# Optimization experiments

Measured on AMD Instinct MI355X. Metric: run time of the kernel, lower is better.

Reference implementation:

```python
import jax, jax.numpy as jnp
import numpy as np
from jax import lax

SR = 16000
N_FFT = 400
HOP = 200
N_MELS = 128
HID = 128


def _mel_fb():
    # torchaudio melscale_fbanks defaults: htk scale, norm=None, f_min=0, f_max=sr/2
    all_freqs = np.linspace(0.0, SR / 2, N_FFT // 2 + 1)  # (201,)
    hz2mel = lambda f: 2595.0 * np.log10(1.0 + f / 700.0)
    mel2hz = lambda m: 700.0 * (10.0 ** (m / 2595.0) - 1.0)
    m_pts = np.linspace(hz2mel(0.0), hz2mel(SR / 2), N_MELS + 2)
    f_pts = mel2hz(m_pts)  # (130,)
    f_diff = np.diff(f_pts)  # (129,)
    slopes = f_pts[None, :] - all_freqs[:, None]  # (201,130)
    down = -slopes[:, :-2] / f_diff[:-1]
    up = slopes[:, 2:] / f_diff[1:]
    fb = np.maximum(0.0, np.minimum(down, up))  # (201,128)
    return jnp.asarray(fb, dtype=jnp.float32)

MEL_FB = _mel_fb()
HANN = jnp.asarray(np.hanning(N_FFT + 1)[:-1], dtype=jnp.float32)  # periodic hann(400)


def mel_spectrogram(x):
    # x: (B, T) waveform -> (B, n_mels, frames), power=2 mel spectrogram
    pad = N_FFT // 2
    xp = jnp.pad(x, ((0, 0), (pad, pad)), mode='reflect')
    n_frames = 1 + (xp.shape[1] - N_FFT) // HOP  # 81 for T=16000
    idx = jnp.arange(n_frames)[:, None] * HOP + jnp.arange(N_FFT)[None, :]
    frames = xp[:, idx] * HANN  # (B, frames, 400)
    spec = jnp.fft.rfft(frames, axis=-1)  # (B, frames, 201)
    power = jnp.abs(spec) ** 2
    mel = power @ MEL_FB  # (B, frames, 128)
    return jnp.transpose(mel, (0, 2, 1))  # (B, 128, frames)


def lstm_layer(x, W, U, b):
    # x: (B, T, F); gate order i, f, g, o (matches torch slicing)
    B = x.shape[0]
    h0 = jnp.zeros((B, HID), x.dtype)
    c0 = jnp.zeros((B, HID), x.dtype)

    def step(carry, x_t):
        h, c = carry
        gates = x_t @ W + h @ U + b  # (B, 4H)
        i = jax.nn.sigmoid(gates[:, :HID])
        f = jax.nn.sigmoid(gates[:, HID:2 * HID])
        g = jnp.tanh(gates[:, 2 * HID:3 * HID])
        o = jax.nn.sigmoid(gates[:, 3 * HID:])
        c = f * c + i * g
        h = o * jnp.tanh(c)
        return (h, c), h

    _, hs = lax.scan(step, (h0, c0), jnp.transpose(x, (1, 0, 2)))  # (T, B, H)
    return jnp.transpose(hs, (1, 0, 2))  # (B, T, H)


def setup_inputs() -> dict:
    key = jax.random.key(0)
    ks = jax.random.split(key, 16)
    s = 0.05
    return {
        'x': jax.random.normal(ks[0], (1024, 16000), dtype=jnp.float32),
        'conv_w': jax.random.normal(ks[1], (128, 128, 3), dtype=jnp.float32) * s,  # (out,in,k)
        'conv_b': jax.random.normal(ks[2], (128,), dtype=jnp.float32) * s,
        'W1': jax.random.normal(ks[3], (128, 4 * HID), dtype=jnp.float32) * s,
        'U1': jax.random.normal(ks[4], (HID, 4 * HID), dtype=jnp.float32) * s,
        'b1': jax.random.normal(ks[5], (4 * HID,), dtype=jnp.float32) * s,
        'W2': jax.random.normal(ks[6], (HID, 4 * HID), dtype=jnp.float32) * s,
        'U2': jax.random.normal(ks[7], (HID, 4 * HID), dtype=jnp.float32) * s,
        'b2': jax.random.normal(ks[8], (4 * HID,), dtype=jnp.float32) * s,
        'fc1_w': jax.random.normal(ks[9], (128, 128), dtype=jnp.float32) * s,  # (in,out)
        'fc1_b': jax.random.normal(ks[10], (128,), dtype=jnp.float32) * s,
        'proj_w': jax.random.normal(ks[11], (128, 35), dtype=jnp.float32) * s,  # (in,out)
        'proj_b': jax.random.normal(ks[12], (35,), dtype=jnp.float32) * s,
    }


def reference(x, conv_w, conv_b, W1, U1, b1, W2, U2, b2, fc1_w, fc1_b, proj_w, proj_b):
    # MelSpectrogram -> Conv1d(128,128,3) -> permute -> LSTM x2 -> fc1 -> mean(time) -> proj
    spec = mel_spectrogram(x)  # (B, 128, 81)
    conv = lax.conv_general_dilated(
        spec, conv_w, window_strides=(1,), padding='VALID',
        dimension_numbers=('NCH', 'OIH', 'NCH')) + conv_b[None, :, None]  # (B,128,79)
    h = jnp.transpose(conv, (0, 2, 1))  # (B, 79, 128)
    h = lstm_layer(h, W1, U1, b1)
    h = lstm_layer(h, W2, U2, b2)
    h = h @ fc1_w + fc1_b  # (B, 79, 128)
    h = jnp.mean(h, axis=1)  # (B, 128)
    return h @ proj_w + proj_b  # (B, 35)
```

## Files before the change

### kernel.cpp

```cpp
#include <hip/hip_runtime.h>
#include <math.h>

#define PI_D 3.14159265358979323846

#define BATCH   1024
#define TLEN    16000
#define NFFT    400
#define HOP     200
#define NFRAME  81
#define NBIN    201
#define NMEL    128
#define HID     128
#define TSTEPS  79
#define GATES   512

#define KDFT    416
#define NDFT    512
#define SINOFF  256
#define KPOW    224
#define KCONV   384
#define NCHUNK  2
#define CHROWS  (BATCH*NFRAME/NCHUNK)

static inline size_t al512(size_t v){ return (v + 511) & ~((size_t)511); }

__device__ __forceinline__ unsigned short bf_rne(float f){
    unsigned u = __float_as_uint(f);
    u += 0x7FFF + ((u >> 16) & 1);
    return (unsigned short)(u >> 16);
}
__device__ __forceinline__ void bf_split(float f, unsigned short& h, unsigned short& l){
    h = bf_rne(f);
    float hf = __uint_as_float(((unsigned)h) << 16);
    l = bf_rne(f - hf);
}
__device__ __forceinline__ void bf_split_fast(float f, unsigned short& h, unsigned short& l){
    unsigned u = __float_as_uint(f);
    h = (unsigned short)(u >> 16);
    float hf = __uint_as_float(u & 0xFFFF0000u);
    l = (unsigned short)(__float_as_uint(f - hf) >> 16);
}

__device__ __forceinline__ int kswz(int n, int k){
    return (k & ~31) | (((((k >> 3) & 3) ^ ((n >> 1) & 3))) << 3) | (k & 7);
}

typedef short bf16x8 __attribute__((ext_vector_type(8)));
typedef float f32x4  __attribute__((ext_vector_type(4)));
typedef unsigned short us8 __attribute__((ext_vector_type(8)));
typedef unsigned short us4 __attribute__((ext_vector_type(4)));
typedef _Float16 f16x8 __attribute__((ext_vector_type(8)));

__device__ __forceinline__ void gld16(const unsigned short* g, unsigned short* l){
    __builtin_amdgcn_global_load_lds(
        (const __attribute__((address_space(1))) unsigned int*)g,
        (__attribute__((address_space(3))) unsigned int*)l, 16, 0, 0);
}

__global__ void setup_dft_t(unsigned short* __restrict__ th, unsigned short* __restrict__ tl){
    int idx = blockIdx.x*256 + threadIdx.x;
    if (idx >= NDFT*KDFT) return;
    int n = idx / KDFT, k = idx % KDFT;
    double v = 0.0;
    if (k < 400) {
        double w = 0.5 - 0.5*cos(2.0*PI_D*(double)k/400.0);
        if (n < NBIN)                              v = w * cos(2.0*PI_D*(double)((k*n)%400)/400.0);
        else if (n >= SINOFF && n < SINOFF + NBIN) v = w * sin(2.0*PI_D*(double)((k*(n-SINOFF))%400)/400.0);
    }
    unsigned short h, l; bf_split((float)v, h, l);
    int o = n*KDFT + kswz(n, k);
    th[o] = h; tl[o] = l;
}

__global__ void setup_fb_t(unsigned short* __restrict__ fh, unsigned short* __restrict__ fl){
    int idx = blockIdx.x*256 + threadIdx.x;
    if (idx >= NMEL*KPOW) return;
    int m = idx / KPOW, f = idx % KPOW;
    float v = 0.f;
    if (f < NBIN) {
        double melmax = 2595.0 * log10(1.0 + 8000.0/700.0);
        double p0 = 700.0*(pow(10.0, melmax*(double)(m  )/129.0/2595.0) - 1.0);
        double p1 = 700.0*(pow(10.0, melmax*(double)(m+1)/129.0/2595.0) - 1.0);
        double p2 = 700.0*(pow(10.0, melmax*(double)(m+2)/129.0/2595.0) - 1.0);
        double freq = 40.0 * (double)f;
        double dn = (freq - p0)/(p1 - p0);
        double up = (p2 - freq)/(p2 - p1);
        double t  = dn < up ? dn : up;
        if (t < 0.0) t = 0.0;
        v = (float)t;
    }
    unsigned short h, l; bf_split(v, h, l);
    int o = m*KPOW + kswz(m, f);
    fh[o] = h; fl[o] = l;
}

__global__ void setup_wc_t(unsigned short* __restrict__ wh, unsigned short* __restrict__ wl,
                           const float* __restrict__ cw){
    int idx = blockIdx.x*256 + threadIdx.x;
    if (idx >= NMEL*KCONV) return;
    int o = idx / KCONV, kk = idx % KCONV;
    int ksh = kk >> 7, i = kk & 127;
    unsigned short h, l; bf_split(cw[o*384 + i*3 + ksh], h, l);
    int p = o*KCONV + kswz(o, kk);
    wh[p] = h; wl[p] = l;
}

__global__ void setup_w_t(unsigned short* __restrict__ wh, unsigned short* __restrict__ wl,
                          const float* __restrict__ w){
    int idx = blockIdx.x*256 + threadIdx.x;
    if (idx >= GATES*HID) return;
    int c = idx / HID, i = idx % HID;
    unsigned short h, l; bf_split(w[(size_t)i*GATES + c], h, l);
    int p = c*HID + kswz(c, i);
    wh[p] = h; wl[p] = l;
}

__global__ void setup_comb(float* __restrict__ cwm, float* __restrict__ cb,
                           const float* __restrict__ fc1w, const float* __restrict__ fc1b,
                           const float* __restrict__ projw, const float* __restrict__ projb){
    int idx = blockIdx.x*256 + threadIdx.x;
    if (idx < 128*64) {
        int i = idx / 64, o = idx % 64;
        float v = 0.f;
        if (o < 35) {
            double s = 0.0;
            for (int m = 0; m < 128; m++) s += (double)fc1w[i*128+m] * (double)projw[m*35+o];
            v = (float)s;
        }
        cwm[idx] = v;
    } else if (idx < 128*64 + 64) {
        int o = idx - 128*64;
        float v = 0.f;
        if (o < 35) {
            double s = (double)projb[o];
            for (int m = 0; m < 128; m++) s += (double)fc1b[m] * (double)projw[m*35+o];
            v = (float)s;
        }
        cb[o] = v;
    }
}

__global__ void setup_uf(_Float16* __restrict__ uf, const float* __restrict__ u){
    int idx = blockIdx.x*256 + threadIdx.x;
    if (idx >= 65536) return;
    int j    = idx & 7;
    int lane = (idx >> 3) & 63;
    int nt   = (idx >> 9) & 3;
    int ks   = (idx >> 11) & 3;
    int w    = (idx >> 13) & 7;
    int k = ks*32 + (lane >> 4)*8 + j;
    int c = w*64 + nt*16 + (lane & 15);
    uf[idx] = (_Float16)u[(size_t)k*GATES + c];
}

enum AMode { A_NORMAL=0, A_FRAMES=1, A_POWER=2, A_CONV3=3 };

template<int AMODE, bool BIAS, int NT>
__global__ __launch_bounds__(256)
void mgemm_k(const float* __restrict__ A,
             const unsigned short* __restrict__ BTh, const unsigned short* __restrict__ BTl,
             const float* __restrict__ bias, float* __restrict__ C,
             int Ksteps, int lda, int kstride, int ldc,
             const float* __restrict__ aux, int rowbase)
{
    __shared__ unsigned short Ash[2][128][32], Asl[2][128][32];
    __shared__ unsigned short Bsh[2][128][32], Bsl[2][128][32];

    const int nwg = gridDim.x;
    const int qq = nwg >> 3, rmd = nwg & 7;
    const int xcd = blockIdx.x & 7, loc = blockIdx.x >> 3;
    const int swz = (xcd < rmd ? xcd*(qq+1) : rmd*(qq+1) + (xcd - rmd)*qq) + loc;
    constexpr int LGNT = (NT == 4) ? 2 : 0;
    const int m0 = (swz >> LGNT) * 128;
    const int n0 = (swz & (NT-1)) * 128;

    const int tid = threadIdx.x;
    const int lane = tid & 63, w = tid >> 6;
    const int wr = (w >> 1) * 64, wc = (w & 1) * 64;
    const int l15 = lane & 15;
    const int swf = ((lane & 15) >> 1) & 3;
    const int pos = (((lane >> 4) ^ swf) << 3);

    const int sr  = tid >> 3;
    const int wcol = (((((tid & 7) >> 1)) ^ ((tid >> 4) & 3)) << 3) + ((tid & 1) << 2);

    float va0[16], vb0[16], va1[16], vb1[16];

    auto issue_loads = [&](float (&va)[16], float (&vb)[16], int ksn){
        const int k0n = ksn * 32;
        #pragma unroll
        for (int p = 0; p < 4; p++) {
            const int row = p*32 + sr;
            const int kk = k0n + (tid & 7)*4;
            if constexpr (AMODE == A_NORMAL) {
                *(float4*)&va[p*4] = *(const float4*)(A + (size_t)(m0+row)*lda + kk);
            } else if constexpr (AMODE == A_POWER) {
                const float* src = A + (size_t)(m0+row)*lda + kk;
                *(float4*)&va[p*4] = *(const float4*)(src);
                *(float4*)&vb[p*4] = *(const float4*)(src + SINOFF);
            } else if constexpr (AMODE == A_FRAMES) {
                const int rr = rowbase + m0 + row;
                const int b = rr / NFRAME, f = rr - b*NFRAME;
                const float* xb = aux + (size_t)b * TLEN;
                const int q0 = f*HOP + kk - 200;
                if (q0 >= 0 && q0 + 3 < TLEN) {
                    *(float4*)&va[p*4] = *(const float4*)(xb + q0);
                } else {
                    #pragma unroll
                    for (int j = 0; j < 4; j++) {
                        int q = q0 + j;
                        if (q < 0) q = -q;
                        else if (q >= TLEN) q = 2*TLEN - 2 - q;
                        va[p*4+j] = xb[q];
                    }
                }
            } else {
                const int rr = m0 + row;
                const int b = rr / TSTEPS, t = rr - b*TSTEPS;
                const int ksh = kk >> 7, i = kk & 127;
                *(float4*)&va[p*4] = *(const float4*)(aux + ((size_t)(b*NFRAME + t + ksh)*NMEL + i));
            }
        }
        (void)vb;
    };
    auto write_stage = [&](float (&va)[16], float (&vb)[16], int wb){
        #pragma unroll
        for (int p = 0; p < 4; p++) {
            const int row = p*32 + sr;
            us4 hv, lv;
            #pragma unroll
            for (int j = 0; j < 4; j++) {
                float f = va[p*4+j];
                if constexpr (AMODE == A_POWER) f = f*f + vb[p*4+j]*vb[p*4+j];
                unsigned short h, l; bf_split_fast(f, h, l);
                hv[j] = h; lv[j] = l;
            }
            *(us4*)&Ash[wb][row][wcol] = hv;
            *(us4*)&Asl[wb][row][wcol] = lv;
        }
        (void)vb;
    };
    auto dma_b = [&](int wb, int ksn){
        const int k0n = ksn * 32;
        #pragma unroll
        for (int p = 0; p < 2; p++) {
            const size_t o = (size_t)(n0 + p*64 + w*16 + (lane >> 2))*kstride + k0n + (lane & 3)*8;
            gld16(BTh + o, &Bsh[wb][p*64 + w*16][0]);
            gld16(BTl + o, &Bsl[wb][p*64 + w*16][0]);
        }
    };

    f32x4 acc[4][4] = {};

    issue_loads(va1, vb1, 0);
    dma_b(0, 0);
    write_stage(va1, vb1, 0);
    issue_loads(va0, vb0, 1);
    __syncthreads();

    auto iter = [&](int ks, float (&vac)[16], float (&vbc)[16],
                    float (&vao)[16], float (&vbo)[16], int bufc){
        const bool pf1 = (ks + 1 < Ksteps);
        const bool pf2 = (ks + 2 < Ksteps);
        if (pf2) issue_loads(vao, vbo, ks + 2);
        if (pf1) dma_b(bufc ^ 1, ks + 1);

        bf16x8 ah[4], al[4];
        #pragma unroll
        for (int mt = 0; mt < 4; mt++) {
            ah[mt] = *(const bf16x8*)&Ash[bufc][wr + mt*16 + l15][pos];
            al[mt] = *(const bf16x8*)&Asl[bufc][wr + mt*16 + l15][pos];
        }
        #pragma unroll
        for (int nt = 0; nt < 4; nt++) {
            const int nr = wc + nt*16 + l15;
            bf16x8 bh = *(const bf16x8*)&Bsh[bufc][nr][pos];
            bf16x8 bl = *(const bf16x8*)&Bsl[bufc][nr][pos];
            #pragma unroll
            for (int mt = 0; mt < 4; mt++) {
                acc[mt][nt] = __builtin_amdgcn_mfma_f32_16x16x32_bf16(ah[mt], bh, acc[mt][nt], 0, 0, 0);
                acc[mt][nt] = __builtin_amdgcn_mfma_f32_16x16x32_bf16(ah[mt], bl, acc[mt][nt], 0, 0, 0);
                acc[mt][nt] = __builtin_amdgcn_mfma_f32_16x16x32_bf16(al[mt], bh, acc[mt][nt], 0, 0, 0);
            }
        }

        if (pf1) {
            write_stage(vac, vbc, bufc ^ 1);
            __syncthreads();
        }
    };

    for (int ks = 0; ks < Ksteps; ks += 2) {
        iter(ks, va0, vb0, va1, vb1, 0);
        if (ks + 1 < Ksteps) iter(ks + 1, va1, vb1, va0, vb0, 1);
    }

    const int quad = lane >> 4;
    #pragma unroll
    for (int nt = 0; nt < 4; nt++) {
        const int col = n0 + wc + (nt << 4) + l15;
        float b = 0.f;
        if constexpr (BIAS) b = bias[col];
        #pragma unroll
        for (int mt = 0; mt < 4; mt++) {
            #pragma unroll
            for (int r = 0; r < 4; r++) {
                const int row = m0 + wr + (mt << 4) + quad*4 + r;
                C[(size_t)row*ldc + col] = acc[mt][nt][r] + b;
            }
        }
    }
}

__global__ __launch_bounds__(256)
void gemm_small(const float* __restrict__ A, const float* __restrict__ Bm,
                const float* __restrict__ bias, float* __restrict__ C,
                int M, int N, int K, int lda, int ldb, int ldc)
{
    __shared__ float As[16][64+4];
    __shared__ float Bs[16][64];
    const int tid = threadIdx.x;
    const int tx = tid & 15, ty = tid >> 4;
    const int m0 = blockIdx.x * 64;
    float acc[4][4] = {{0,0,0,0},{0,0,0,0},{0,0,0,0},{0,0,0,0}};
    const int am = tid >> 2, ak = (tid & 3) * 4;
    const int bk = tid >> 4, bn = (tid & 15) * 4;
    for (int k0 = 0; k0 < K; k0 += 16) {
        float4 av = *(const float4*)(A + (size_t)(m0+am)*lda + k0 + ak);
        As[ak+0][am]=av.x; As[ak+1][am]=av.y; As[ak+2][am]=av.z; As[ak+3][am]=av.w;
        *(float4*)&Bs[bk][bn] = *(const float4*)(Bm + (size_t)(k0+bk)*ldb + bn);
        __syncthreads();
        #pragma unroll
        for (int k = 0; k < 16; k++) {
            float4 a = *(const float4*)&As[k][ty*4];
            float4 b = *(const float4*)&Bs[k][tx*4];
            #pragma unroll
            for (int i = 0; i < 4; i++) {
                float av_ = ((const float*)&a)[i];
                acc[i][0] = fmaf(av_, b.x, acc[i][0]);
                acc[i][1] = fmaf(av_, b.y, acc[i][1]);
                acc[i][2] = fmaf(av_, b.z, acc[i][2]);
                acc[i][3] = fmaf(av_, b.w, acc[i][3]);
            }
        }
        __syncthreads();
    }
    #pragma unroll
    for (int ir = 0; ir < 4; ir++) {
        const int row = m0 + ty*4 + ir;
        #pragma unroll
        for (int jc = 0; jc < 4; jc++) {
            const int col = tx*4 + jc;
            if (col < N) C[(size_t)row*ldc + col] = acc[ir][jc] + bias[col];
        }
    }
}

__device__ __forceinline__ float sigm_f(float x){ return 1.f/(1.f + __expf(-x)); }
__device__ __forceinline__ float tanh_f(float x){ float e = __expf(2.f*x); return 1.f - 2.f/(e + 1.f); }

#define LROWS 4
#define LTHREADS 512
#define HPAD 136

__global__ __launch_bounds__(LTHREADS, 2)
void lstm_k(const float* __restrict__ X, const _Float16* __restrict__ Uf, float* __restrict__ H)
{
    __shared__ _Float16 hsA[16*HPAD];
    __shared__ float gs[GATES*5];
    const int tid = threadIdx.x;
    const int b0 = blockIdx.x * LROWS;
    const int lane = tid & 63, w = tid >> 6;
    const int m16 = lane & 15, quad = lane >> 4;
    const int r = tid >> 7;
    const int j = tid & 127;

    f32x4 bfr[4][4];
    #pragma unroll
    for (int ks = 0; ks < 4; ks++)
        #pragma unroll
        for (int nt = 0; nt < 4; nt++) {
            bfr[ks][nt] = *(const f32x4*)(Uf + ((((w*4 + ks)*4 + nt)*64 + lane) << 3));
            asm volatile("" : "+v"(bfr[ks][nt]));
        }

    for (int i = tid; i < 16*HPAD; i += LTHREADS) hsA[i] = (_Float16)0.f;
    float cst = 0.f;
    const float* xb = X + ((size_t)(b0 + r)*TSTEPS)*GATES + j;
    __syncthreads();

    float xi = xb[0], xf = xb[128], xg = xb[256], xo = xb[384];

    for (int t = 0; t < TSTEPS; t++) {
        float xi_n = 0.f, xf_n = 0.f, xg_n = 0.f, xo_n = 0.f;
        if (t + 1 < TSTEPS) {
            const float* xp = xb + (size_t)(t + 1)*GATES;
            xi_n = xp[0]; xf_n = xp[128]; xg_n = xp[256]; xo_n = xp[384];
        }

        f16x8 ah[4];
        #pragma unroll
        for (int ks = 0; ks < 4; ks++)
            ah[ks] = *(const f16x8*)&hsA[m16*HPAD + ks*32 + quad*8];

        f32x4 acc[4] = {{0,0,0,0},{0,0,0,0},{0,0,0,0},{0,0,0,0}};
        #pragma unroll
        for (int ks = 0; ks < 4; ks++)
            #pragma unroll
            for (int nt = 0; nt < 4; nt++)
                acc[nt] = __builtin_amdgcn_mfma_f32_16x16x32_f16(
                    ah[ks], __builtin_bit_cast(f16x8, bfr[ks][nt]), acc[nt], 0, 0, 0);

        if (quad == 0) {
            #pragma unroll
            for (int nt = 0; nt < 4; nt++) {
                const int c = w*64 + nt*16 + m16;
                #pragma unroll
                for (int rr = 0; rr < 4; rr++) gs[c*5 + rr] = acc[nt][rr];
            }
        }
        __syncthreads();

        {
            const float gi = gs[(      j)*5 + r] + xi;
            const float gf = gs[(128 + j)*5 + r] + xf;
            const float gg = gs[(256 + j)*5 + r] + xg;
            const float go = gs[(384 + j)*5 + r] + xo;
            const float cn = sigm_f(gf)*cst + sigm_f(gi)*tanh_f(gg);
            cst = cn;
            const float hn = sigm_f(go)*tanh_f(cn);
            H[((size_t)(b0 + r)*TSTEPS + t)*HID + j] = hn;
            hsA[r*HPAD + j] = (_Float16)hn;
        }
        __syncthreads();

        xi = xi_n; xf = xf_n; xg = xg_n; xo = xo_n;
    }
}

__global__ void mean_k(const float* __restrict__ H, float* __restrict__ Mh){
    const int idx = blockIdx.x*256 + threadIdx.x;
    if (idx >= BATCH*HID) return;
    const int b = idx >> 7, j = idx & 127;
    const float* p = H + (size_t)b*TSTEPS*HID + j;
    float s = 0.f;
    for (int t = 0; t < TSTEPS; t++) s += p[(size_t)t*HID];
    Mh[idx] = s * (1.0f/(float)TSTEPS);
}

extern "C" void kernel_launch(void* const* d_in, const int* in_sizes, int n_in,
                              void* d_out, int out_size, void* d_ws, size_t ws_size,
                              hipStream_t stream)
{
    const float* x      = (const float*)d_in[0];
    const float* conv_w = (const float*)d_in[1];
    const float* conv_b = (const float*)d_in[2];
    const float* W1     = (const float*)d_in[3];
    const float* U1     = (const float*)d_in[4];
    const float* b1     = (const float*)d_in[5];
    const float* W2     = (const float*)d_in[6];
    const float* U2     = (const float*)d_in[7];
    const float* b2     = (const float*)d_in[8];
    const float* fc1_w  = (const float*)d_in[9];
    const float* fc1_b  = (const float*)d_in[10];
    const float* proj_w = (const float*)d_in[11];
    const float* proj_b = (const float*)d_in[12];
    float* out = (float*)d_out;

    char* ws = (char*)d_ws;
    size_t off = 0;
    unsigned short* Tth = (unsigned short*)(ws + off); off = al512(off + (size_t)NDFT*KDFT*2);
    unsigned short* Ttl = (unsigned short*)(ws + off); off = al512(off + (size_t)NDFT*KDFT*2);
    unsigned short* fbh = (unsigned short*)(ws + off); off = al512(off + (size_t)NMEL*KPOW*2);
    unsigned short* fbl = (unsigned short*)(ws + off); off = al512(off + (size_t)NMEL*KPOW*2);
    unsigned short* wch = (unsigned short*)(ws + off); off = al512(off + (size_t)NMEL*KCONV*2);
    unsigned short* wcl = (unsigned short*)(ws + off); off = al512(off + (size_t)NMEL*KCONV*2);
    unsigned short* w1h = (unsigned short*)(ws + off); off = al512(off + (size_t)GATES*HID*2);
    unsigned short* w1l = (unsigned short*)(ws + off); off = al512(off + (size_t)GATES*HID*2);
    unsigned short* w2h = (unsigned short*)(ws + off); off = al512(off + (size_t)GATES*HID*2);
    unsigned short* w2l = (unsigned short*)(ws + off); off = al512(off + (size_t)GATES*HID*2);
    float* Cw   = (float*)(ws + off); off = al512(off + (size_t)128*64*4);
    float* Cb   = (float*)(ws + off); off = al512(off + (size_t)64*4);
    float* Mh   = (float*)(ws + off); off = al512(off + (size_t)BATCH*HID*4);
    _Float16* Uf1 = (_Float16*)(ws + off); off = al512(off + (size_t)65536*2);
    _Float16* Uf2 = (_Float16*)(ws + off); off = al512(off + (size_t)65536*2);
    float* MEL  = (float*)(ws + off); off = al512(off + (size_t)BATCH*NFRAME*NMEL*4);
    float* CONV = (float*)(ws + off); off = al512(off + (size_t)BATCH*TSTEPS*NMEL*4);
    float* X    = (float*)(ws + off); off = al512(off + (size_t)BATCH*TSTEPS*GATES*4);
    float* DFT = X;
    float* H1  = MEL;
    float* H2  = CONV;
    (void)ws_size; (void)out_size; (void)n_in; (void)in_sizes;

    setup_dft_t<<<(NDFT*KDFT + 255)/256, 256, 0, stream>>>(Tth, Ttl);
    setup_fb_t <<<(NMEL*KPOW + 255)/256, 256, 0, stream>>>(fbh, fbl);
    setup_wc_t <<<(NMEL*KCONV + 255)/256, 256, 0, stream>>>(wch, wcl, conv_w);
    setup_w_t  <<<(GATES*HID + 255)/256, 256, 0, stream>>>(w1h, w1l, W1);
    setup_w_t  <<<(GATES*HID + 255)/256, 256, 0, stream>>>(w2h, w2l, W2);
    setup_comb <<<(128*64 + 64 + 255)/256, 256, 0, stream>>>(Cw, Cb, fc1_w, fc1_b, proj_w, proj_b);
    setup_uf   <<<65536/256, 256, 0, stream>>>(Uf1, U1);
    setup_uf   <<<65536/256, 256, 0, stream>>>(Uf2, U2);

    for (int ch = 0; ch < NCHUNK; ch++) {
        const int rowbase = ch * CHROWS;
        mgemm_k<A_FRAMES,false,4><<<(CHROWS/128)*4, 256, 0, stream>>>(
            nullptr, Tth, Ttl, nullptr, DFT, KDFT/32, 0, KDFT, NDFT, x, rowbase);
        mgemm_k<A_POWER,false,1><<<CHROWS/128, 256, 0, stream>>>(
            DFT, fbh, fbl, nullptr, MEL + (size_t)rowbase*NMEL, KPOW/32, NDFT, KPOW, NMEL, nullptr, 0);
    }

    mgemm_k<A_CONV3,true,1><<<BATCH*TSTEPS/128, 256, 0, stream>>>(
        nullptr, wch, wcl, conv_b, CONV, KCONV/32, 0, KCONV, NMEL, MEL, 0);

    mgemm_k<A_NORMAL,true,4><<<(BATCH*TSTEPS/128)*4, 256, 0, stream>>>(
        CONV, w1h, w1l, b1, X, HID/32, NMEL, HID, GATES, nullptr, 0);
    lstm_k<<<BATCH/LROWS, LTHREADS, 0, stream>>>(X, Uf1, H1);

    mgemm_k<A_NORMAL,true,4><<<(BATCH*TSTEPS/128)*4, 256, 0, stream>>>(
        H1, w2h, w2l, b2, X, HID/32, HID, HID, GATES, nullptr, 0);
    lstm_k<<<BATCH/LROWS, LTHREADS, 0, stream>>>(X, Uf2, H2);

    mean_k<<<(BATCH*HID + 255)/256, 256, 0, stream>>>(H2, Mh);
    gemm_small<<<BATCH/64, 256, 0, stream>>>(Mh, Cw, Cb, out, BATCH, 35, HID, HID, 64, 35);
}
```

Before: 677.7 us.

## Split 400-point DFT into two 200-point DFTs with twiddle recombination

Replaces the direct windowed 400-point real DFT GEMM with a radix-2 decimation: the windowed frame is split into even and odd samples, each transformed by a 200-point DFT matrix (K=224, N=256). The two half-spectra are then recombined with twiddle factors inside the power-loading stage of the mel GEMM. This roughly halves the DFT GEMM FLOPs and the B-matrix size. In exchange it adds scalar strided gathers of waveform samples, no longer vectorized, and irregular scalar loads with twiddle arithmetic in the power stage.

```diff
diff --git a/kernel.cpp b/kernel.cpp
--- a/kernel.cpp
+++ b/kernel.cpp
@@ -14,9 +14,9 @@
 #define TSTEPS  79
 #define GATES   512
 
-#define KDFT    416
-#define NDFT    512
-#define SINOFF  256
+#define KDFT2   224
+#define NDFT2   256
+#define SINOFF2 128
 #define KPOW    224
 #define KCONV   384
 #define NCHUNK  2
@@ -57,19 +57,41 @@
         (__attribute__((address_space(3))) unsigned int*)l, 16, 0, 0);
 }
 
-__global__ void setup_dft_t(unsigned short* __restrict__ th, unsigned short* __restrict__ tl){
+__global__ void setup_dft2_t(unsigned short* __restrict__ th, unsigned short* __restrict__ tl){
     int idx = blockIdx.x*256 + threadIdx.x;
-    if (idx >= NDFT*KDFT) return;
-    int n = idx / KDFT, k = idx % KDFT;
+    if (idx >= NDFT2*KDFT2) return;
+    int c = idx / KDFT2, j = idx % KDFT2;
     double v = 0.0;
-    if (k < 400) {
-        double w = 0.5 - 0.5*cos(2.0*PI_D*(double)k/400.0);
-        if (n < NBIN)                              v = w * cos(2.0*PI_D*(double)((k*n)%400)/400.0);
-        else if (n >= SINOFF && n < SINOFF + NBIN) v = w * sin(2.0*PI_D*(double)((k*(n-SINOFF))%400)/400.0);
+    if (j < 200) {
+        if (c <= 100)
+            v = cos(2.0*PI_D*(double)((j*c)%200)/200.0);
+        else if (c >= SINOFF2+1 && c <= SINOFF2+99)
+            v = sin(2.0*PI_D*(double)((j*(c-SINOFF2))%200)/200.0);
     }
     unsigned short h, l; bf_split((float)v, h, l);
-    int o = n*KDFT + kswz(n, k);
+    int o = c*KDFT2 + kswz(c, j);
     th[o] = h; tl[o] = l;
+}
+
+__global__ void setup_wt(float* __restrict__ wt){
+    int i = blockIdx.x*256 + threadIdx.x;
+    if (i < 448) {
+        int p = i / 224, j = i % 224;
+        float v = 0.f;
+        if (j < 200) {
+            double k = 2.0*(double)j + (double)p;
+            v = (float)(0.5 - 0.5*cos(2.0*PI_D*k/400.0));
+        }
+        wt[i] = v;
+    } else if (i < 896) {
+        int n = (i - 448) >> 1;
+        float v = 0.f;
+        if (n <= 200) {
+            double a = PI_D*(double)n/200.0;
+            v = (float)(((i - 448) & 1) ? sin(a) : cos(a));
+        }
+        wt[i] = v;
+    }
 }
 
 __global__ void setup_fb_t(unsigned short* __restrict__ fh, unsigned short* __restrict__ fl){
@@ -161,7 +183,8 @@
              const unsigned short* __restrict__ BTh, const unsigned short* __restrict__ BTl,
              const float* __restrict__ bias, float* __restrict__ C,
              int Ksteps, int lda, int kstride, int ldc,
-             const float* __restrict__ aux, int rowbase)
+             const float* __restrict__ aux, int rowbase,
+             const float* __restrict__ aux2)
 {
     __shared__ unsigned short Ash[2][128][32], Asl[2][128][32];
     __shared__ unsigned short Bsh[2][128][32], Bsl[2][128][32];
@@ -170,7 +193,7 @@
     const int qq = nwg >> 3, rmd = nwg & 7;
     const int xcd = blockIdx.x & 7, loc = blockIdx.x >> 3;
     const int swz = (xcd < rmd ? xcd*(qq+1) : rmd*(qq+1) + (xcd - rmd)*qq) + loc;
-    constexpr int LGNT = (NT == 4) ? 2 : 0;
+    constexpr int LGNT = (NT == 4) ? 2 : (NT == 2) ? 1 : 0;
     const int m0 = (swz >> LGNT) * 128;
     const int n0 = (swz & (NT-1)) * 128;
 
@@ -184,9 +207,9 @@
     const int sr  = tid >> 3;
     const int wcol = (((((tid & 7) >> 1)) ^ ((tid >> 4) & 3)) << 3) + ((tid & 1) << 2);
 
-    float va0[16], vb0[16], va1[16], vb1[16];
-
-    auto issue_loads = [&](float (&va)[16], float (&vb)[16], int ksn){
+    float va0[16], va1[16];
+
+    auto issue_loads = [&](float (&va)[16], int ksn){
         const int k0n = ksn * 32;
         #pragma unroll
         for (int p = 0; p < 4; p++) {
@@ -195,24 +218,39 @@
             if constexpr (AMODE == A_NORMAL) {
                 *(float4*)&va[p*4] = *(const float4*)(A + (size_t)(m0+row)*lda + kk);
             } else if constexpr (AMODE == A_POWER) {
-                const float* src = A + (size_t)(m0+row)*lda + kk;
-                *(float4*)&va[p*4] = *(const float4*)(src);
-                *(float4*)&vb[p*4] = *(const float4*)(src + SINOFF);
+                const float* srcE = A + (size_t)(m0+row)*lda;
+                const float* srcO = srcE + NDFT2;
+                #pragma unroll
+                for (int t = 0; t < 4; t++) {
+                    const int n = kk + t;
+                    float v_ = 0.f;
+                    if (n <= 200) {
+                        int mm; float s;
+                        if (n <= 100)      { mm = n;       s = -1.f; }
+                        else if (n < 200)  { mm = 200 - n; s =  1.f; }
+                        else               { mm = 0;       s = -1.f; }
+                        const float Er  = srcE[mm], Ei = s * srcE[SINOFF2 + mm];
+                        const float Or_ = srcO[mm], Oi = s * srcO[SINOFF2 + mm];
+                        const float tr = aux2[448 + 2*n], ti = aux2[448 + 2*n + 1];
+                        const float Yr = Er + tr*Or_ + ti*Oi;
+                        const float Yi = Ei + tr*Oi - ti*Or_;
+                        v_ = Yr*Yr + Yi*Yi;
+                    }
+                    va[p*4 + t] = v_;
+                }
             } else if constexpr (AMODE == A_FRAMES) {
-                const int rr = rowbase + m0 + row;
-                const int b = rr / NFRAME, f = rr - b*NFRAME;
+                const int hh = rowbase + m0 + row;
+                const int fg = hh >> 1, pp = hh & 1;
+                const int b = fg / NFRAME, f = fg - b*NFRAME;
                 const float* xb = aux + (size_t)b * TLEN;
-                const int q0 = f*HOP + kk - 200;
-                if (q0 >= 0 && q0 + 3 < TLEN) {
-                    *(float4*)&va[p*4] = *(const float4*)(xb + q0);
-                } else {
-                    #pragma unroll
-                    for (int j = 0; j < 4; j++) {
-                        int q = q0 + j;
-                        if (q < 0) q = -q;
-                        else if (q >= TLEN) q = 2*TLEN - 2 - q;
-                        va[p*4+j] = xb[q];
-                    }
+                const int q0 = f*HOP - 200 + pp + 2*kk;
+                float4 wv = *(const float4*)(aux2 + pp*224 + kk);
+                #pragma unroll
+                for (int t = 0; t < 4; t++) {
+                    int q = q0 + 2*t;
+                    if (q < 0) q = -q;
+                    else if (q >= TLEN) q = 2*TLEN - 2 - q;
+                    va[p*4 + t] = xb[q] * ((const float*)&wv)[t];
                 }
             } else {
                 const int rr = m0 + row;
@@ -221,24 +259,20 @@
                 *(float4*)&va[p*4] = *(const float4*)(aux + ((size_t)(b*NFRAME + t + ksh)*NMEL + i));
             }
         }
-        (void)vb;
     };
-    auto write_stage = [&](float (&va)[16], float (&vb)[16], int wb){
+    auto write_stage = [&](float (&va)[16], int wb){
         #pragma unroll
         for (int p = 0; p < 4; p++) {
             const int row = p*32 + sr;
             us4 hv, lv;
             #pragma unroll
             for (int j = 0; j < 4; j++) {
-                float f = va[p*4+j];
-                if constexpr (AMODE == A_POWER) f = f*f + vb[p*4+j]*vb[p*4+j];
-                unsigned short h, l; bf_split_fast(f, h, l);
+                unsigned short h, l; bf_split_fast(va[p*4+j], h, l);
                 hv[j] = h; lv[j] = l;
             }
             *(us4*)&Ash[wb][row][wcol] = hv;
             *(us4*)&Asl[wb][row][wcol] = lv;
         }
-        (void)vb;
     };
     auto dma_b = [&](int wb, int ksn){
         const int k0n = ksn * 32;
@@ -252,17 +286,16 @@
 
     f32x4 acc[4][4] = {};
 
-    issue_loads(va1, vb1, 0);
+    issue_loads(va1, 0);
     dma_b(0, 0);
-    write_stage(va1, vb1, 0);
-    issue_loads(va0, vb0, 1);
+    write_stage(va1, 0);
+    issue_loads(va0, 1);
     __syncthreads();
 
-    auto iter = [&](int ks, float (&vac)[16], float (&vbc)[16],
-                    float (&vao)[16], float (&vbo)[16], int bufc){
+    auto iter = [&](int ks, float (&vac)[16], float (&vao)[16], int bufc){
         const bool pf1 = (ks + 1 < Ksteps);
         const bool pf2 = (ks + 2 < Ksteps);
-        if (pf2) issue_loads(vao, vbo, ks + 2);
+        if (pf2) issue_loads(vao, ks + 2);
         if (pf1) dma_b(bufc ^ 1, ks + 1);
 
         bf16x8 ah[4], al[4];
@@ -285,14 +318,14 @@
         }
 
         if (pf1) {
-            write_stage(vac, vbc, bufc ^ 1);
+            write_stage(vac, bufc ^ 1);
             __syncthreads();
         }
     };
 
     for (int ks = 0; ks < Ksteps; ks += 2) {
-        iter(ks, va0, vb0, va1, vb1, 0);
-        if (ks + 1 < Ksteps) iter(ks + 1, va1, vb1, va0, vb0, 1);
+        iter(ks, va0, va1, 0);
+        if (ks + 1 < Ksteps) iter(ks + 1, va1, va0, 1);
     }
 
     const int quad = lane >> 4;
@@ -469,8 +502,8 @@
 
     char* ws = (char*)d_ws;
     size_t off = 0;
-    unsigned short* Tth = (unsigned short*)(ws + off); off = al512(off + (size_t)NDFT*KDFT*2);
-    unsigned short* Ttl = (unsigned short*)(ws + off); off = al512(off + (size_t)NDFT*KDFT*2);
+    unsigned short* Tth = (unsigned short*)(ws + off); off = al512(off + (size_t)NDFT2*KDFT2*2);
+    unsigned short* Ttl = (unsigned short*)(ws + off); off = al512(off + (size_t)NDFT2*KDFT2*2);
     unsigned short* fbh = (unsigned short*)(ws + off); off = al512(off + (size_t)NMEL*KPOW*2);
     unsigned short* fbl = (unsigned short*)(ws + off); off = al512(off + (size_t)NMEL*KPOW*2);
     unsigned short* wch = (unsigned short*)(ws + off); off = al512(off + (size_t)NMEL*KCONV*2);
@@ -481,6 +514,7 @@
     unsigned short* w2l = (unsigned short*)(ws + off); off = al512(off + (size_t)GATES*HID*2);
     float* Cw   = (float*)(ws + off); off = al512(off + (size_t)128*64*4);
     float* Cb   = (float*)(ws + off); off = al512(off + (size_t)64*4);
+    float* wt   = (float*)(ws + off); off = al512(off + (size_t)896*4);
     float* Mh   = (float*)(ws + off); off = al512(off + (size_t)BATCH*HID*4);
     _Float16* Uf1 = (_Float16*)(ws + off); off = al512(off + (size_t)65536*2);
     _Float16* Uf2 = (_Float16*)(ws + off); off = al512(off + (size_t)65536*2);
@@ -492,7 +526,8 @@
     float* H2  = CONV;
     (void)ws_size; (void)out_size; (void)n_in; (void)in_sizes;
 
-    setup_dft_t<<<(NDFT*KDFT + 255)/256, 256, 0, stream>>>(Tth, Ttl);
+    setup_dft2_t<<<(NDFT2*KDFT2 + 255)/256, 256, 0, stream>>>(Tth, Ttl);
+    setup_wt   <<<4, 256, 0, stream>>>(wt);
     setup_fb_t <<<(NMEL*KPOW + 255)/256, 256, 0, stream>>>(fbh, fbl);
     setup_wc_t <<<(NMEL*KCONV + 255)/256, 256, 0, stream>>>(wch, wcl, conv_w);
     setup_w_t  <<<(GATES*HID + 255)/256, 256, 0, stream>>>(w1h, w1l, W1);
@@ -503,21 +538,21 @@
 
     for (int ch = 0; ch < NCHUNK; ch++) {
         const int rowbase = ch * CHROWS;
-        mgemm_k<A_FRAMES,false,4><<<(CHROWS/128)*4, 256, 0, stream>>>(
-            nullptr, Tth, Ttl, nullptr, DFT, KDFT/32, 0, KDFT, NDFT, x, rowbase);
+        mgemm_k<A_FRAMES,false,2><<<(2*CHROWS/128)*2, 256, 0, stream>>>(
+            nullptr, Tth, Ttl, nullptr, DFT, KDFT2/32, 0, KDFT2, NDFT2, x, 2*rowbase, wt);
         mgemm_k<A_POWER,false,1><<<CHROWS/128, 256, 0, stream>>>(
-            DFT, fbh, fbl, nullptr, MEL + (size_t)rowbase*NMEL, KPOW/32, NDFT, KPOW, NMEL, nullptr, 0);
+            DFT, fbh, fbl, nullptr, MEL + (size_t)rowbase*NMEL, KPOW/32, 2*NDFT2, KPOW, NMEL, nullptr, 0, wt);
     }
 
     mgemm_k<A_CONV3,true,1><<<BATCH*TSTEPS/128, 256, 0, stream>>>(
-        nullptr, wch, wcl, conv_b, CONV, KCONV/32, 0, KCONV, NMEL, MEL, 0);
+        nullptr, wch, wcl, conv_b, CONV, KCONV/32, 0, KCONV, NMEL, MEL, 0, nullptr);
 
     mgemm_k<A_NORMAL,true,4><<<(BATCH*TSTEPS/128)*4, 256, 0, stream>>>(
-        CONV, w1h, w1l, b1, X, HID/32, NMEL, HID, GATES, nullptr, 0);
+        CONV, w1h, w1l, b1, X, HID/32, NMEL, HID, GATES, nullptr, 0, nullptr);
     lstm_k<<<BATCH/LROWS, LTHREADS, 0, stream>>>(X, Uf1, H1);
 
     mgemm_k<A_NORMAL,true,4><<<(BATCH*TSTEPS/128)*4, 256, 0, stream>>>(
-        H1, w2h, w2l, b2, X, HID/32, HID, HID, GATES, nullptr, 0);
+        H1, w2h, w2l, b2, X, HID/32, HID, HID, GATES, nullptr, 0, nullptr);
     lstm_k<<<BATCH/LROWS, LTHREADS, 0, stream>>>(X, Uf2, H2);
 
     mean_k<<<(BATCH*HID + 255)/256, 256, 0, stream>>>(H2, Mh);
```

After: 709.0 us. 1.05x slower.
